# Performance work log

Measured on AMD Instinct MI355X. Metric: run time of the kernel, lower is better.

## Reference

```python
import jax, jax.numpy as jnp
import numpy as np
import math

B, S, E = 4, 2048, 1024

def setup_inputs() -> dict:
    key = jax.random.key(0)
    ks = jax.random.split(key, 12)
    scale = 1.0 / math.sqrt(E)
    inp = {
        "query": jax.random.normal(ks[0], (B, S, E), jnp.float32),
        "key_": jax.random.normal(ks[1], (B, S, E), jnp.float32),
        "value": jax.random.normal(ks[2], (B, S, E), jnp.float32),
        # causal mask, broadcast over batch: 1 = keep, 0 = mask
        "mask": jnp.broadcast_to(jnp.tril(jnp.ones((S, S), jnp.int32)), (B, S, S)),
        "Wq": jax.random.uniform(ks[3], (E, E), jnp.float32, -scale, scale),
        "bq": jax.random.uniform(ks[4], (E,), jnp.float32, -scale, scale),
        "Wk": jax.random.uniform(ks[5], (E, E), jnp.float32, -scale, scale),
        "bk": jax.random.uniform(ks[6], (E,), jnp.float32, -scale, scale),
        "Wv": jax.random.uniform(ks[7], (E, E), jnp.float32, -scale, scale),
        "bv": jax.random.uniform(ks[8], (E,), jnp.float32, -scale, scale),
        "Wo": jax.random.uniform(ks[9], (E, E), jnp.float32, -scale, scale),
        "bo": jax.random.uniform(ks[10], (E,), jnp.float32, -scale, scale),
    }
    return inp

def reference(query, key_, value, mask, Wq, bq, Wk, bk, Wv, bv, Wo, bo):
    # Linear projections (torch Linear: x @ W.T + b)
    Q = jnp.einsum('bse,fe->bsf', query, Wq) + bq
    K = jnp.einsum('bse,fe->bsf', key_, Wk) + bk
    V = jnp.einsum('bse,fe->bsf', value, Wv) + bv
    # NOTE: module never splits heads; scores over full embed_dim, scaled by sqrt(embed_dim)
    scores = jnp.einsum('bqe,bke->bqk', Q, K) / jnp.sqrt(jnp.asarray(E, Q.dtype))
    scores = jnp.where(mask == 0, -jnp.inf, scores)
    attn = jax.nn.softmax(scores, axis=-1)
    attn_out = jnp.einsum('bqk,bke->bqe', attn, V)
    return jnp.einsum('bse,fe->bsf', attn_out, Wo) + bo
```

## Files before the change

### kernel.cpp

```cpp
#include <hip/hip_runtime.h>

typedef __bf16 bf16;
typedef __attribute__((ext_vector_type(8))) __bf16 bf16x8;
typedef __attribute__((ext_vector_type(4))) __bf16 bf16x4;
typedef __attribute__((ext_vector_type(2))) __bf16 bf16x2;
typedef __attribute__((ext_vector_type(4))) float f32x4;

#define DEVINL __device__ __forceinline__

DEVINL void gload_lds16(const bf16* g, bf16* l) {
    __builtin_amdgcn_global_load_lds(
        (__attribute__((address_space(1))) unsigned int*)(unsigned long long)g,
        (__attribute__((address_space(3))) unsigned int*)l,
        16, 0, 0);
}

DEVINL void xcd_swizzle(int& bx, int& by) {
    const int gx = gridDim.x, gy = gridDim.y;
    const int l = blockIdx.y * gx + blockIdx.x;
    const int xcd = l & 7;
    const int li = l >> 3;
    by = xcd * (gy >> 3) + li / gx;
    bx = li - (li / gx) * gx;
}

DEVINL void xcd_swizzle_bal(int& bx, int& by) {
    const int gx = gridDim.x, gy = gridDim.y;
    const int l = blockIdx.y * gx + blockIdx.x;
    const int xcd = l & 7;
    const int li = l >> 3;
    const int j = li / gx;
    bx = li - j * gx;
    by = j ? (gy - 1 - xcd) : xcd;
}

__global__ __launch_bounds__(256) void cvt3_f32_to_bf16(
    const float* __restrict__ a, const float* __restrict__ b,
    const float* __restrict__ c, bf16* __restrict__ out, int n4) {
    int i = blockIdx.x * blockDim.x + threadIdx.x;
    if (i >= n4) return;
    const float* src = (blockIdx.z == 0) ? a : (blockIdx.z == 1) ? b : c;
    bf16* dst = out + (size_t)blockIdx.z * (size_t)n4 * 4;
    float4 f = ((const float4*)src)[i];
    bf16x4 o;
    o.x = (bf16)f.x; o.y = (bf16)f.y; o.z = (bf16)f.z; o.w = (bf16)f.w;
    ((bf16x4*)dst)[i] = o;
}

__global__ __launch_bounds__(256) void cvt4_f32_to_bf16(
    const float* __restrict__ a, const float* __restrict__ b,
    const float* __restrict__ c, const float* __restrict__ d,
    bf16* __restrict__ out, int n4) {
    int i = blockIdx.x * blockDim.x + threadIdx.x;
    if (i >= n4) return;
    const float* src = (blockIdx.z == 0) ? a : (blockIdx.z == 1) ? b
                     : (blockIdx.z == 2) ? c : d;
    bf16* dst = out + (size_t)blockIdx.z * (size_t)n4 * 4;
    float4 f = ((const float4*)src)[i];
    bf16x4 o;
    o.x = (bf16)f.x; o.y = (bf16)f.y; o.z = (bf16)f.z; o.w = (bf16)f.w;
    ((bf16x4*)dst)[i] = o;
}

__global__ __launch_bounds__(256) void transpose_bf16(
    const unsigned short* __restrict__ in, unsigned short* __restrict__ out,
    int R, int C) {
    __shared__ unsigned short t[64][65];
    const size_t bo = (size_t)blockIdx.z * R * C;
    const int r0 = blockIdx.y * 64, c0 = blockIdx.x * 64;
#pragma unroll
    for (int i = 0; i < 16; i++) {
        int lin = threadIdx.x + i * 256;
        int r = lin >> 6, c = lin & 63;
        t[r][c] = in[bo + (size_t)(r0 + r) * C + (c0 + c)];
    }
    __syncthreads();
#pragma unroll
    for (int i = 0; i < 16; i++) {
        int lin = threadIdx.x + i * 256;
        int r = lin >> 6, c = lin & 63;
        out[bo + (size_t)(c0 + r) * R + (r0 + c)] = t[c][r];
    }
}

__global__ __launch_bounds__(256) void bias_fold(
    const float* __restrict__ Wo, const float* __restrict__ bv,
    const float* __restrict__ bo, float* __restrict__ bout) {
    const int e = blockIdx.x * 4 + (threadIdx.x >> 6);
    const int lane = threadIdx.x & 63;
    float s = 0.f;
    for (int k = lane; k < 1024; k += 64) s += Wo[e * 1024 + k] * bv[k];
#pragma unroll
    for (int off = 32; off > 0; off >>= 1) s += __shfl_xor(s, off, 64);
    if (lane == 0) bout[e] = s + bo[e];
}

template <int EPI>
__global__ __launch_bounds__(256) void gemm_bt128(
    const bf16* __restrict__ A, const bf16* __restrict__ B,
    const float* __restrict__ bias0, const float* __restrict__ bias1,
    const float* __restrict__ bias2, void* __restrict__ Cv,
    int M, int N, int K,
    long long sA, long long sB, long long sC,
    float scale) {
    int bx, by;
    xcd_swizzle(bx, by);
    const int bz = blockIdx.z;
    const int m0 = by * 128, n0 = bx * 128;

    A += (size_t)bz * sA;
    B += (size_t)bz * sB;
    const float* bias = (bz == 0) ? bias0 : (bz == 1) ? bias1 : bias2;

    __shared__ __align__(16) bf16 As[2][128 * 32];
    __shared__ __align__(16) bf16 Bs[2][128 * 32];

    const int tid = threadIdx.x;
    const int wave = tid >> 6;
    const int lane = tid & 63;
    const int lr = lane & 15;
    const int lq = lane >> 4;
    const int wm = (wave >> 1) * 64;
    const int wn = (wave & 1) * 64;
    const int srow = lane >> 2;
    const int scol = ((lane & 3) ^ ((lane >> 3) & 3)) * 8;

    const bf16* gA = A + (size_t)(m0 + wave * 16 + srow) * K + scol;
    const bf16* gB = B + (size_t)(n0 + wave * 16 + srow) * K + scol;
    const size_t rowskip = (size_t)64 * K;
    const int rsw = (lq ^ ((lr >> 1) & 3)) * 8;

    f32x4 acc[4][4];
    const f32x4 fzero = {0.f, 0.f, 0.f, 0.f};
#pragma unroll
    for (int i = 0; i < 4; i++)
#pragma unroll
        for (int j = 0; j < 4; j++) acc[i][j] = fzero;

#define STAGE128(bufi)                                          \
    do {                                                        \
        gload_lds16(gA,           As[bufi] + wave * 512);       \
        gload_lds16(gA + rowskip, As[bufi] + (wave + 4) * 512); \
        gload_lds16(gB,           Bs[bufi] + wave * 512);       \
        gload_lds16(gB + rowskip, Bs[bufi] + (wave + 4) * 512); \
        gA += 32; gB += 32;                                     \
    } while (0)

    STAGE128(0);
    int cur = 0;
    for (int k0 = 0; k0 < K; k0 += 32) {
        __syncthreads();
        if (k0 + 32 < K) STAGE128(cur ^ 1);

        bf16x8 af[4], bfr[4];
#pragma unroll
        for (int i = 0; i < 4; i++)
            af[i] = *(const bf16x8*)(As[cur] + (wm + i * 16 + lr) * 32 + rsw);
#pragma unroll
        for (int j = 0; j < 4; j++)
            bfr[j] = *(const bf16x8*)(Bs[cur] + (wn + j * 16 + lr) * 32 + rsw);
#pragma unroll
        for (int i = 0; i < 4; i++)
#pragma unroll
            for (int j = 0; j < 4; j++)
                acc[i][j] = __builtin_amdgcn_mfma_f32_16x16x32_bf16(
                    af[i], bfr[j], acc[i][j], 0, 0, 0);
        cur ^= 1;
    }
#undef STAGE128

#pragma unroll
    for (int j = 0; j < 4; j++) {
        const int col = n0 + wn + j * 16 + lr;
        const float bb = bias ? bias[col] : 0.0f;
#pragma unroll
        for (int i = 0; i < 4; i++) {
            const int rowb = m0 + wm + i * 16 + lq * 4;
#pragma unroll
            for (int r = 0; r < 4; r++) {
                if (EPI == 0)
                    ((bf16*)Cv)[(size_t)bz * sC + (size_t)(rowb + r) * N + col] =
                        (bf16)(acc[i][j][r] * scale + bb);
                else
                    ((float*)Cv)[(size_t)bz * sC + (size_t)(rowb + r) * N + col] =
                        acc[i][j][r] * scale + bb;
            }
        }
    }
}

template <int EPI>
__global__ __launch_bounds__(512) void gemm_pipe(
    const bf16* __restrict__ A, const bf16* __restrict__ B,
    const float* __restrict__ bias0, const float* __restrict__ bias1,
    const float* __restrict__ bias2, void* __restrict__ Cv,
    int M, int N, int K,
    long long sA, long long sB, long long sC,
    float scale, int causal) {
    int bx, by;
    if (causal) xcd_swizzle_bal(bx, by);
    else        xcd_swizzle(bx, by);
    const int bz = blockIdx.z;
    const int m0 = by * 128, n0 = bx * 256;
    if (causal == 1 && n0 > m0 + 127) return;
    const int NT = K >> 5;

    A += (size_t)bz * sA;
    B += (size_t)bz * sB;
    const float* bias = (bz == 0) ? bias0 : (bz == 1) ? bias1 : bias2;

    __shared__ __align__(16) bf16 As[4][128 * 32];
    __shared__ __align__(16) bf16 Bs[4][256 * 32];

    const int tid = threadIdx.x;
    const int wave = tid >> 6;
    const int lane = tid & 63;
    const int lr = lane & 15;
    const int lq = lane >> 4;
    const int wm = (wave >> 2) * 64;
    const int wn = (wave & 3) * 64;

    const int srow = lane >> 2;
    const int scol = ((lane & 3) ^ ((lane >> 3) & 3)) * 8;
    const bf16* gA  = A + (size_t)(m0 + wave * 16 + srow) * K + scol;
    const bf16* gB0 = B + (size_t)(n0 + wave * 32 + srow) * K + scol;
    const size_t rowskip = (size_t)16 * K;

    const int rsw = (lq ^ ((lr >> 1) & 3)) * 8;

    f32x4 acc[4][4];
    const f32x4 fzero = {0.f, 0.f, 0.f, 0.f};
#pragma unroll
    for (int i = 0; i < 4; i++)
#pragma unroll
        for (int j = 0; j < 4; j++) acc[i][j] = fzero;

#define STAGEP(bufi, koff)                                               \
    do {                                                                 \
        gload_lds16(gA + (koff),            As[bufi] + wave * 512);      \
        gload_lds16(gB0 + (koff),           Bs[bufi] + wave * 1024);     \
        gload_lds16(gB0 + rowskip + (koff), Bs[bufi] + wave * 1024 + 512); \
    } while (0)

    STAGEP(0, 0);
    STAGEP(1, 32);
    STAGEP(2, 64);
    asm volatile("s_waitcnt vmcnt(6)" ::: "memory");
    __builtin_amdgcn_s_barrier();

    for (int t = 0; t < NT; ++t) {
        const int bfi = t & 3;

        bf16x8 af[4], bfr[4];
#pragma unroll
        for (int i = 0; i < 4; i++)
            af[i] = *(const bf16x8*)(As[bfi] + (wm + i * 16 + lr) * 32 + rsw);
#pragma unroll
        for (int j = 0; j < 4; j++)
            bfr[j] = *(const bf16x8*)(Bs[bfi] + (wn + j * 16 + lr) * 32 + rsw);

        if (t + 3 < NT) STAGEP((t + 3) & 3, (t + 3) * 32);

        const int rem = NT - 1 - t;
        if (rem >= 3)      asm volatile("s_waitcnt vmcnt(6)" ::: "memory");
        else if (rem == 2) asm volatile("s_waitcnt vmcnt(3)" ::: "memory");
        else if (rem == 1) asm volatile("s_waitcnt vmcnt(0)" ::: "memory");
        __builtin_amdgcn_s_barrier();
        __builtin_amdgcn_sched_barrier(0);

        __builtin_amdgcn_s_setprio(1);
#pragma unroll
        for (int i = 0; i < 4; i++)
#pragma unroll
            for (int j = 0; j < 4; j++)
                acc[i][j] = __builtin_amdgcn_mfma_f32_16x16x32_bf16(
                    af[i], bfr[j], acc[i][j], 0, 0, 0);
        __builtin_amdgcn_s_setprio(0);
        __builtin_amdgcn_s_barrier();
    }
#undef STAGEP

#pragma unroll
    for (int j = 0; j < 4; j++) {
        const int col = n0 + wn + j * 16 + lr;
        const float bb = bias ? bias[col] : 0.0f;
#pragma unroll
        for (int i = 0; i < 4; i++) {
            const int rowb = m0 + wm + i * 16 + lq * 4;
#pragma unroll
            for (int r = 0; r < 4; r++) {
                if (EPI == 0)
                    ((bf16*)Cv)[(size_t)bz * sC + (size_t)(rowb + r) * N + col] =
                        (bf16)(acc[i][j][r] * scale + bb);
                else
                    ((float*)Cv)[(size_t)bz * sC + (size_t)(rowb + r) * N + col] =
                        acc[i][j][r] * scale + bb;
            }
        }
    }
}

__global__ __launch_bounds__(256, 2) void gemm_pv128(
    const bf16* __restrict__ A, const bf16* __restrict__ B,
    const float* __restrict__ bias, float* __restrict__ C,
    int M, int N, int K,
    long long sA, long long sB, long long sC,
    float scale) {
    int bx, by;
    xcd_swizzle_bal(bx, by);
    const int bz = blockIdx.z;
    const int m0 = by * 128, n0 = bx * 128;
    int Keff = m0 + 128; if (Keff > K) Keff = K;
    const int NT = Keff >> 5;

    A += (size_t)bz * sA;
    B += (size_t)bz * sB;

    __shared__ __align__(16) bf16 As[4][128 * 32];
    __shared__ __align__(16) bf16 Bs[4][128 * 32];

    const int tid = threadIdx.x;
    const int wave = tid >> 6;
    const int lane = tid & 63;
    const int lr = lane & 15;
    const int lq = lane >> 4;
    const int wm = (wave >> 1) * 64;
    const int wn = (wave & 1) * 64;

    const int srow = lane >> 2;
    const int scol = ((lane & 3) ^ ((lane >> 3) & 3)) * 8;
    const bf16* gA = A + (size_t)(m0 + wave * 16 + srow) * K + scol;
    const bf16* gB = B + (size_t)(n0 + wave * 16 + srow) * K + scol;
    const size_t rowskip = (size_t)64 * K;

    const int rsw = (lq ^ ((lr >> 1) & 3)) * 8;

    f32x4 acc[4][4];
    const f32x4 fzero = {0.f, 0.f, 0.f, 0.f};
#pragma unroll
    for (int i = 0; i < 4; i++)
#pragma unroll
        for (int j = 0; j < 4; j++) acc[i][j] = fzero;

#define STAGEV(bufi, koff)                                                 \
    do {                                                                   \
        gload_lds16(gA + (koff),           As[bufi] + wave * 512);         \
        gload_lds16(gA + rowskip + (koff), As[bufi] + (wave + 4) * 512);   \
        gload_lds16(gB + (koff),           Bs[bufi] + wave * 512);         \
        gload_lds16(gB + rowskip + (koff), Bs[bufi] + (wave + 4) * 512);   \
    } while (0)

    STAGEV(0, 0);
    STAGEV(1, 32);
    STAGEV(2, 64);
    asm volatile("s_waitcnt vmcnt(8)" ::: "memory");
    __builtin_amdgcn_s_barrier();

    for (int t = 0; t < NT; ++t) {
        const int bfi = t & 3;

        bf16x8 af[4], bfr[4];
#pragma unroll
        for (int i = 0; i < 4; i++)
            af[i] = *(const bf16x8*)(As[bfi] + (wm + i * 16 + lr) * 32 + rsw);
#pragma unroll
        for (int j = 0; j < 4; j++)
            bfr[j] = *(const bf16x8*)(Bs[bfi] + (wn + j * 16 + lr) * 32 + rsw);

        if (t + 3 < NT) STAGEV((t + 3) & 3, (t + 3) * 32);

        const int rem = NT - 1 - t;
        if (rem >= 3)      asm volatile("s_waitcnt vmcnt(8)" ::: "memory");
        else if (rem == 2) asm volatile("s_waitcnt vmcnt(4)" ::: "memory");
        else if (rem == 1) asm volatile("s_waitcnt vmcnt(0)" ::: "memory");
        __builtin_amdgcn_s_barrier();
        __builtin_amdgcn_sched_barrier(0);

        __builtin_amdgcn_s_setprio(1);
#pragma unroll
        for (int i = 0; i < 4; i++)
#pragma unroll
            for (int j = 0; j < 4; j++)
                acc[i][j] = __builtin_amdgcn_mfma_f32_16x16x32_bf16(
                    af[i], bfr[j], acc[i][j], 0, 0, 0);
        __builtin_amdgcn_s_setprio(0);
        __builtin_amdgcn_s_barrier();
    }
#undef STAGEV

#pragma unroll
    for (int j = 0; j < 4; j++) {
        const int col = n0 + wn + j * 16 + lr;
        const float bb = bias[col];
#pragma unroll
        for (int i = 0; i < 4; i++) {
            const int rowb = m0 + wm + i * 16 + lq * 4;
#pragma unroll
            for (int r = 0; r < 4; r++)
                C[(size_t)bz * sC + (size_t)(rowb + r) * N + col] =
                    acc[i][j][r] * scale + bb;
        }
    }
}

__global__ __launch_bounds__(256) void softmax_causal(
    const bf16* __restrict__ Sc, bf16* __restrict__ P, int S) {
    const int row = blockIdx.x;
    const int q = row & (S - 1);
    const bf16* src = Sc + (size_t)row * S;
    bf16* dst = P + (size_t)row * S;
    const int L = q + 1;
    const int tid = threadIdx.x;
    const int k0 = tid * 8;

    bf16x8 u = ((const bf16x8*)src)[tid];
    float v[8];
    float mx = -3.0e38f;
#pragma unroll
    for (int i = 0; i < 8; i++) {
        v[i] = (k0 + i < L) ? (float)u[i] : -3.0e38f;
        mx = fmaxf(mx, v[i]);
    }
#pragma unroll
    for (int off = 32; off > 0; off >>= 1) mx = fmaxf(mx, __shfl_xor(mx, off, 64));
    __shared__ float redm[4], reds[4];
    if ((tid & 63) == 0) redm[tid >> 6] = mx;
    __syncthreads();
    mx = fmaxf(fmaxf(redm[0], redm[1]), fmaxf(redm[2], redm[3]));

    float sum = 0.f;
#pragma unroll
    for (int i = 0; i < 8; i++) {
        float e = (v[i] > -1.0e38f) ? __expf(v[i] - mx) : 0.f;
        v[i] = e;
        sum += e;
    }
#pragma unroll
    for (int off = 32; off > 0; off >>= 1) sum += __shfl_xor(sum, off, 64);
    if ((tid & 63) == 0) reds[tid >> 6] = sum;
    __syncthreads();
    sum = reds[0] + reds[1] + reds[2] + reds[3];
    const float inv = 1.0f / sum;
    bf16x8 o;
#pragma unroll
    for (int i = 0; i < 8; i++) o[i] = (bf16)(v[i] * inv);
    ((bf16x8*)dst)[tid] = o;
}

extern "C" void kernel_launch(void* const* d_in, const int* in_sizes, int n_in,
                              void* d_out, int out_size, void* d_ws, size_t ws_size,
                              hipStream_t stream) {
    const int B = 4, S = 2048, E = 1024;
    const size_t SBE = (size_t)B * S * E;
    const size_t EE = (size_t)E * E;

    const float* q_in = (const float*)d_in[0];
    const float* k_in = (const float*)d_in[1];
    const float* v_in = (const float*)d_in[2];
    const float* Wq = (const float*)d_in[4];
    const float* bq = (const float*)d_in[5];
    const float* Wk = (const float*)d_in[6];
    const float* bk = (const float*)d_in[7];
    const float* Wv = (const float*)d_in[8];
    const float* bv = (const float*)d_in[9];
    const float* Wo = (const float*)d_in[10];
    const float* bo = (const float*)d_in[11];

    char* ws = (char*)d_ws;
    bf16* qkvb = (bf16*)ws;
    bf16* Sc = (bf16*)ws;
    bf16* WvT = (bf16*)(ws + 3 * SBE * 2);
    float* bout = (float*)(ws + 3 * SBE * 2 + EE * 2);
    char* p = ws + (size_t)B * S * S * 4;
    bf16* QKVb = (bf16*)p; p += 3 * SBE * 2;
    bf16* VWt = (bf16*)p; p += SBE * 2;
    bf16* Pb = (bf16*)p; p += (size_t)B * S * S * 2;
    bf16* Wb = (bf16*)p; p += 4 * EE * 2;

    bf16* Qb = QKVb;
    bf16* Kb = QKVb + SBE;
    bf16* VW = QKVb + 2 * SBE;
    bf16* Wob = Wb + 3 * EE;
    bf16* Wvo = Wb + 2 * EE;

    dim3 blk(256), blk512(512);

    dim3 gcvt3((int)(SBE / 4 / 256), 1, 3);
    cvt3_f32_to_bf16<<<gcvt3, blk, 0, stream>>>(q_in, k_in, v_in, qkvb, (int)(SBE / 4));
    dim3 gcvt4((int)(EE / 4 / 256), 1, 4);
    cvt4_f32_to_bf16<<<gcvt4, blk, 0, stream>>>(Wq, Wk, Wv, Wo, Wb, (int)(EE / 4));

    dim3 gtw(16, 16, 1);
    transpose_bf16<<<gtw, blk, 0, stream>>>((const unsigned short*)(Wb + 2 * EE),
                                            (unsigned short*)WvT, E, E);
    dim3 gwvo(E / 128, E / 128, 1);
    gemm_bt128<0><<<gwvo, blk, 0, stream>>>(Wob, WvT, nullptr, nullptr, nullptr,
                                            Wvo, E, E, E, 0, 0, 0, 1.f);
    bias_fold<<<256, blk, 0, stream>>>(Wo, bv, bo, bout);

    dim3 gproj(E / 256, (B * S) / 128, 3);
    gemm_pipe<0><<<gproj, blk512, 0, stream>>>(qkvb, Wb, bq, bk, nullptr, QKVb,
                                               B * S, E, E,
                                               (long long)SBE, (long long)EE,
                                               (long long)SBE, 1.f, 0);

    dim3 gt(E / 64, S / 64, B);
    transpose_bf16<<<gt, blk, 0, stream>>>((const unsigned short*)VW,
                                           (unsigned short*)VWt, S, E);

    dim3 gsc(S / 256, S / 128, B);
    gemm_pipe<0><<<gsc, blk512, 0, stream>>>(Qb, Kb, nullptr, nullptr, nullptr, Sc,
                                             S, S, E,
                                             (long long)S * E, (long long)S * E,
                                             (long long)S * S, 0.03125f, 1);

    softmax_causal<<<B * S, blk, 0, stream>>>(Sc, Pb, S);

    dim3 gpv(E / 128, S / 128, B);
    gemm_pv128<<<gpv, blk, 0, stream>>>(Pb, VWt, bout, (float*)d_out, S, E, S,
                                        (long long)S * S, (long long)E * S,
                                        (long long)S * E, 1.f);
}
```

Baseline: 394.8 us.

## Replace 128x256 GEMM with 256x256 tile, 8-wave ping-pong schedule, vectorize transpose

The projection and score GEMMs move from a 128x256 tile with a 4-stage K=32 pipeline to a 256x256 tile with K=64 double buffering. Each wave now computes a 128x64 sub-tile in quadrant phases, with loads interleaved between barrier-separated MFMA blocks. The aim is more data reuse per LDS byte and better overlap of global-to-LDS copies with MFMA work. The causal launch drops the balanced XCD swizzle, which may hurt load balance, and the larger tile raises register and LDS pressure. The transpose kernel is also changed to use 4-element vector loads and stores.

```diff
diff --git a/kernel.cpp b/kernel.cpp
--- a/kernel.cpp
+++ b/kernel.cpp
@@ -68,18 +68,23 @@
     __shared__ unsigned short t[64][65];
     const size_t bo = (size_t)blockIdx.z * R * C;
     const int r0 = blockIdx.y * 64, c0 = blockIdx.x * 64;
-#pragma unroll
-    for (int i = 0; i < 16; i++) {
-        int lin = threadIdx.x + i * 256;
-        int r = lin >> 6, c = lin & 63;
-        t[r][c] = in[bo + (size_t)(r0 + r) * C + (c0 + c)];
+    const int tr = threadIdx.x >> 4;
+    const int tc = threadIdx.x & 15;
+#pragma unroll
+    for (int i = 0; i < 4; i++) {
+        int r = tr + i * 16;
+        ushort4 v = *(const ushort4*)&in[bo + (size_t)(r0 + r) * C + (c0 + tc * 4)];
+        t[r][tc * 4 + 0] = v.x; t[r][tc * 4 + 1] = v.y;
+        t[r][tc * 4 + 2] = v.z; t[r][tc * 4 + 3] = v.w;
     }
     __syncthreads();
 #pragma unroll
-    for (int i = 0; i < 16; i++) {
-        int lin = threadIdx.x + i * 256;
-        int r = lin >> 6, c = lin & 63;
-        out[bo + (size_t)(c0 + r) * R + (r0 + c)] = t[c][r];
+    for (int i = 0; i < 4; i++) {
+        int r = tr + i * 16;
+        ushort4 v;
+        v.x = t[tc * 4 + 0][r]; v.y = t[tc * 4 + 1][r];
+        v.z = t[tc * 4 + 2][r]; v.w = t[tc * 4 + 3][r];
+        *(ushort4*)&out[bo + (size_t)(c0 + r) * R + (r0 + tc * 4)] = v;
     }
 }
 
@@ -190,7 +195,7 @@
 }
 
 template <int EPI>
-__global__ __launch_bounds__(512) void gemm_pipe(
+__global__ __launch_bounds__(512) void gemm8p(
     const bf16* __restrict__ A, const bf16* __restrict__ B,
     const float* __restrict__ bias0, const float* __restrict__ bias1,
     const float* __restrict__ bias2, void* __restrict__ Cv,
@@ -198,103 +203,166 @@
     long long sA, long long sB, long long sC,
     float scale, int causal) {
     int bx, by;
-    if (causal) xcd_swizzle_bal(bx, by);
+    if (causal) { bx = blockIdx.x; by = blockIdx.y; }
     else        xcd_swizzle(bx, by);
     const int bz = blockIdx.z;
-    const int m0 = by * 128, n0 = bx * 256;
-    if (causal == 1 && n0 > m0 + 127) return;
-    const int NT = K >> 5;
+    const int m0 = by * 256, n0 = bx * 256;
+    if (causal == 1 && n0 > m0 + 255) return;
 
     A += (size_t)bz * sA;
     B += (size_t)bz * sB;
     const float* bias = (bz == 0) ? bias0 : (bz == 1) ? bias1 : bias2;
 
-    __shared__ __align__(16) bf16 As[4][128 * 32];
-    __shared__ __align__(16) bf16 Bs[4][256 * 32];
+    __shared__ __align__(16) bf16 As[2][256 * 64];
+    __shared__ __align__(16) bf16 Bs[2][256 * 64];
 
     const int tid = threadIdx.x;
-    const int wave = tid >> 6;
-    const int lane = tid & 63;
-    const int lr = lane & 15;
-    const int lq = lane >> 4;
-    const int wm = (wave >> 2) * 64;
-    const int wn = (wave & 3) * 64;
-
-    const int srow = lane >> 2;
-    const int scol = ((lane & 3) ^ ((lane >> 3) & 3)) * 8;
-    const bf16* gA  = A + (size_t)(m0 + wave * 16 + srow) * K + scol;
-    const bf16* gB0 = B + (size_t)(n0 + wave * 32 + srow) * K + scol;
-    const size_t rowskip = (size_t)16 * K;
-
-    const int rsw = (lq ^ ((lr >> 1) & 3)) * 8;
-
-    f32x4 acc[4][4];
-    const f32x4 fzero = {0.f, 0.f, 0.f, 0.f};
-#pragma unroll
-    for (int i = 0; i < 4; i++)
-#pragma unroll
-        for (int j = 0; j < 4; j++) acc[i][j] = fzero;
-
-#define STAGEP(bufi, koff)                                               \
-    do {                                                                 \
-        gload_lds16(gA + (koff),            As[bufi] + wave * 512);      \
-        gload_lds16(gB0 + (koff),           Bs[bufi] + wave * 1024);     \
-        gload_lds16(gB0 + rowskip + (koff), Bs[bufi] + wave * 1024 + 512); \
+    const int w  = tid >> 6;
+    const int l  = tid & 63;
+    const int lr = l & 15;
+    const int lq = l >> 4;
+    const int wm = w >> 2;
+    const int wn = w & 3;
+
+    const int x  = lr & 7;
+    const int c0 = ((lq ^ x)) * 8;
+    const int c1 = (((4 | lq) ^ x)) * 8;
+    const int aBase = (wm * 128 + lr) * 64;
+    const int bBase = (wn * 64 + lr) * 64;
+
+    const int srow = w * 8 + (l >> 3);
+    const int scol = ((l & 7) ^ (l >> 3)) * 8;
+    const bf16* gA = A + (size_t)(m0 + srow) * K + scol;
+    const bf16* gB = B + (size_t)(n0 + srow) * K + scol;
+
+    f32x4 acc[8][4];
+    const f32x4 fz = {0.f, 0.f, 0.f, 0.f};
+#pragma unroll
+    for (int i = 0; i < 8; i++)
+#pragma unroll
+        for (int jj = 0; jj < 4; jj++) acc[i][jj] = fz;
+
+    bf16x8 a[8];
+    bf16x8 bb[8];
+
+#define ST_A(b, h, kt)                                                         \
+    do {                                                                       \
+        const bf16* s_ = gA + (size_t)((h) * 128) * K + (size_t)(kt) * 64;     \
+        gload_lds16(s_,                  As[b] + (h) * 8192 + w * 512);        \
+        gload_lds16(s_ + (size_t)64 * K, As[b] + (h) * 8192 + 4096 + w * 512); \
     } while (0)
-
-    STAGEP(0, 0);
-    STAGEP(1, 32);
-    STAGEP(2, 64);
-    asm volatile("s_waitcnt vmcnt(6)" ::: "memory");
-    __builtin_amdgcn_s_barrier();
-
-    for (int t = 0; t < NT; ++t) {
-        const int bfi = t & 3;
-
-        bf16x8 af[4], bfr[4];
-#pragma unroll
-        for (int i = 0; i < 4; i++)
-            af[i] = *(const bf16x8*)(As[bfi] + (wm + i * 16 + lr) * 32 + rsw);
-#pragma unroll
-        for (int j = 0; j < 4; j++)
-            bfr[j] = *(const bf16x8*)(Bs[bfi] + (wn + j * 16 + lr) * 32 + rsw);
-
-        if (t + 3 < NT) STAGEP((t + 3) & 3, (t + 3) * 32);
-
-        const int rem = NT - 1 - t;
-        if (rem >= 3)      asm volatile("s_waitcnt vmcnt(6)" ::: "memory");
-        else if (rem == 2) asm volatile("s_waitcnt vmcnt(3)" ::: "memory");
-        else if (rem == 1) asm volatile("s_waitcnt vmcnt(0)" ::: "memory");
-        __builtin_amdgcn_s_barrier();
-        __builtin_amdgcn_sched_barrier(0);
-
-        __builtin_amdgcn_s_setprio(1);
-#pragma unroll
-        for (int i = 0; i < 4; i++)
-#pragma unroll
-            for (int j = 0; j < 4; j++)
-                acc[i][j] = __builtin_amdgcn_mfma_f32_16x16x32_bf16(
-                    af[i], bfr[j], acc[i][j], 0, 0, 0);
-        __builtin_amdgcn_s_setprio(0);
-        __builtin_amdgcn_s_barrier();
-    }
-#undef STAGEP
-
-#pragma unroll
-    for (int j = 0; j < 4; j++) {
-        const int col = n0 + wn + j * 16 + lr;
-        const float bb = bias ? bias[col] : 0.0f;
-#pragma unroll
-        for (int i = 0; i < 4; i++) {
-            const int rowb = m0 + wm + i * 16 + lq * 4;
-#pragma unroll
-            for (int r = 0; r < 4; r++) {
+#define ST_B(b, h, kt)                                                         \
+    do {                                                                       \
+        const bf16* s_ = gB + (size_t)((h) * 128) * K + (size_t)(kt) * 64;     \
+        gload_lds16(s_,                  Bs[b] + (h) * 8192 + w * 512);        \
+        gload_lds16(s_ + (size_t)64 * K, Bs[b] + (h) * 8192 + 4096 + w * 512); \
+    } while (0)
+#define RD_A(b, q)                                                             \
+    {                                                                          \
+        _Pragma("unroll")                                                      \
+        for (int f = 0; f < 4; ++f) {                                          \
+            a[f * 2 + 0] = *(const bf16x8*)(As[b] + aBase + ((q) * 64 + f * 16) * 64 + c0); \
+            a[f * 2 + 1] = *(const bf16x8*)(As[b] + aBase + ((q) * 64 + f * 16) * 64 + c1); \
+        }                                                                      \
+    }
+#define RD_B(b, p)                                                             \
+    {                                                                          \
+        _Pragma("unroll")                                                      \
+        for (int n = 0; n < 2; ++n) {                                          \
+            bb[((p) * 2 + n) * 2 + 0] = *(const bf16x8*)(Bs[b] + bBase + ((p) * 32 + n * 16) * 64 + c0); \
+            bb[((p) * 2 + n) * 2 + 1] = *(const bf16x8*)(Bs[b] + bBase + ((p) * 32 + n * 16) * 64 + c1); \
+        }                                                                      \
+    }
+#define MM(q, p)                                                               \
+    {                                                                          \
+        __builtin_amdgcn_s_setprio(1);                                         \
+        _Pragma("unroll")                                                      \
+        for (int f = 0; f < 4; ++f) {                                          \
+            _Pragma("unroll")                                                  \
+            for (int n = 0; n < 2; ++n) {                                      \
+                acc[(q) * 4 + f][(p) * 2 + n] = __builtin_amdgcn_mfma_f32_16x16x32_bf16( \
+                    a[f * 2 + 0], bb[((p) * 2 + n) * 2 + 0], acc[(q) * 4 + f][(p) * 2 + n], 0, 0, 0); \
+                acc[(q) * 4 + f][(p) * 2 + n] = __builtin_amdgcn_mfma_f32_16x16x32_bf16( \
+                    a[f * 2 + 1], bb[((p) * 2 + n) * 2 + 1], acc[(q) * 4 + f][(p) * 2 + n], 0, 0, 0); \
+            }                                                                  \
+        }                                                                      \
+        __builtin_amdgcn_s_setprio(0);                                         \
+    }
+#define BAR()                                                                  \
+    {                                                                          \
+        __builtin_amdgcn_sched_barrier(0);                                     \
+        __builtin_amdgcn_s_barrier();                                          \
+        __builtin_amdgcn_sched_barrier(0);                                     \
+    }
+
+    const int NTt = K >> 6;
+    const int NI  = NTt >> 1;
+
+    ST_B(0, 0, 0); ST_B(0, 1, 0);
+    ST_A(0, 0, 0); ST_A(0, 1, 0);
+    ST_B(1, 0, 1); ST_B(1, 1, 1);
+    asm volatile("s_waitcnt vmcnt(4)" ::: "memory");
+    BAR();
+
+    for (int j = 0; j < NI; ++j) {
+        const int vkt = 2 * j + 1, ckt = 2 * j + 2, dkt = 2 * j + 3;
+        const bool dc = ckt < NTt, dd = dkt < NTt;
+
+        RD_A(0, 0) RD_B(0, 0)
+        ST_A(1, 0, vkt);
+        BAR() MM(0, 0) BAR()
+        RD_B(0, 1)
+        ST_A(1, 1, vkt);
+        BAR() MM(0, 1) BAR()
+        RD_A(0, 1)
+        if (dc) ST_B(0, 0, ckt);
+        BAR() MM(1, 1) BAR()
+        if (dc) {
+            ST_B(0, 1, ckt);
+            asm volatile("s_waitcnt vmcnt(4)" ::: "memory");
+        } else {
+            asm volatile("s_waitcnt vmcnt(0)" ::: "memory");
+        }
+        BAR() MM(1, 0) BAR()
+
+        RD_A(1, 0) RD_B(1, 0)
+        if (dc) ST_A(0, 0, ckt);
+        BAR() MM(0, 0) BAR()
+        RD_B(1, 1)
+        if (dc) ST_A(0, 1, ckt);
+        BAR() MM(0, 1) BAR()
+        RD_A(1, 1)
+        if (dd) ST_B(1, 0, dkt);
+        BAR() MM(1, 1) BAR()
+        if (dd) ST_B(1, 1, dkt);
+        if (j + 1 < NI) {
+            if (dd) asm volatile("s_waitcnt vmcnt(4)" ::: "memory");
+            else    asm volatile("s_waitcnt vmcnt(0)" ::: "memory");
+        }
+        BAR() MM(1, 0) BAR()
+    }
+#undef ST_A
+#undef ST_B
+#undef RD_A
+#undef RD_B
+#undef MM
+#undef BAR
+
+#pragma unroll
+    for (int p = 0; p < 4; ++p) {
+        const int col = n0 + wn * 64 + p * 16 + lr;
+        const float bbv = bias ? bias[col] : 0.0f;
+#pragma unroll
+        for (int f = 0; f < 8; ++f) {
+            const int rowb = m0 + wm * 128 + f * 16 + lq * 4;
+#pragma unroll
+            for (int r = 0; r < 4; ++r) {
                 if (EPI == 0)
                     ((bf16*)Cv)[(size_t)bz * sC + (size_t)(rowb + r) * N + col] =
-                        (bf16)(acc[i][j][r] * scale + bb);
+                        (bf16)(acc[f][p][r] * scale + bbv);
                 else
                     ((float*)Cv)[(size_t)bz * sC + (size_t)(rowb + r) * N + col] =
-                        acc[i][j][r] * scale + bb;
+                        acc[f][p][r] * scale + bbv;
             }
         }
     }
@@ -498,21 +566,21 @@
                                             Wvo, E, E, E, 0, 0, 0, 1.f);
     bias_fold<<<256, blk, 0, stream>>>(Wo, bv, bo, bout);
 
-    dim3 gproj(E / 256, (B * S) / 128, 3);
-    gemm_pipe<0><<<gproj, blk512, 0, stream>>>(qkvb, Wb, bq, bk, nullptr, QKVb,
-                                               B * S, E, E,
-                                               (long long)SBE, (long long)EE,
-                                               (long long)SBE, 1.f, 0);
+    dim3 gproj(E / 256, (B * S) / 256, 3);
+    gemm8p<0><<<gproj, blk512, 0, stream>>>(qkvb, Wb, bq, bk, nullptr, QKVb,
+                                            B * S, E, E,
+                                            (long long)SBE, (long long)EE,
+                                            (long long)SBE, 1.f, 0);
 
     dim3 gt(E / 64, S / 64, B);
     transpose_bf16<<<gt, blk, 0, stream>>>((const unsigned short*)VW,
                                            (unsigned short*)VWt, S, E);
 
-    dim3 gsc(S / 256, S / 128, B);
-    gemm_pipe<0><<<gsc, blk512, 0, stream>>>(Qb, Kb, nullptr, nullptr, nullptr, Sc,
-                                             S, S, E,
-                                             (long long)S * E, (long long)S * E,
-                                             (long long)S * S, 0.03125f, 1);
+    dim3 gsc(S / 256, S / 256, B);
+    gemm8p<0><<<gsc, blk512, 0, stream>>>(Qb, Kb, nullptr, nullptr, nullptr, Sc,
+                                          S, S, E,
+                                          (long long)S * E, (long long)S * E,
+                                          (long long)S * S, 0.03125f, 1);
 
     softmax_causal<<<B * S, blk, 0, stream>>>(Sc, Pb, S);
 
```

Measured after the change: 403.3 us. +2.1%, slower.

## Fuse fp32-to-bf16 input conversion into projection GEMM and retile score GEMM

Applied to the files above, without the earlier changes.

Drops the separate conversion kernel for query/key/value and has a new projection GEMM read fp32 activations directly, converting them to bf16 in registers before the LDS store. This removes one full write and re-read of the three bf16 activation tensors. The deep 4-stage 512-thread pipelined GEMM is replaced by simpler double-buffered 256-thread kernels. The score GEMM now uses 128x64 tiles so causal skipping happens at a finer grain. The transpose is vectorised to ushort4, and the workspace layout is reorganised. The risk is that the simpler pipelines, and the synchronous fp32 loads in the projection, hide memory latency less well than the old pipelined kernel.

```diff
diff --git a/kernel.cpp b/kernel.cpp
--- a/kernel.cpp
+++ b/kernel.cpp
@@ -32,19 +32,6 @@
     const int j = li / gx;
     bx = li - j * gx;
     by = j ? (gy - 1 - xcd) : xcd;
-}
-
-__global__ __launch_bounds__(256) void cvt3_f32_to_bf16(
-    const float* __restrict__ a, const float* __restrict__ b,
-    const float* __restrict__ c, bf16* __restrict__ out, int n4) {
-    int i = blockIdx.x * blockDim.x + threadIdx.x;
-    if (i >= n4) return;
-    const float* src = (blockIdx.z == 0) ? a : (blockIdx.z == 1) ? b : c;
-    bf16* dst = out + (size_t)blockIdx.z * (size_t)n4 * 4;
-    float4 f = ((const float4*)src)[i];
-    bf16x4 o;
-    o.x = (bf16)f.x; o.y = (bf16)f.y; o.z = (bf16)f.z; o.w = (bf16)f.w;
-    ((bf16x4*)dst)[i] = o;
 }
 
 __global__ __launch_bounds__(256) void cvt4_f32_to_bf16(
@@ -68,18 +55,23 @@
     __shared__ unsigned short t[64][65];
     const size_t bo = (size_t)blockIdx.z * R * C;
     const int r0 = blockIdx.y * 64, c0 = blockIdx.x * 64;
-#pragma unroll
-    for (int i = 0; i < 16; i++) {
-        int lin = threadIdx.x + i * 256;
-        int r = lin >> 6, c = lin & 63;
-        t[r][c] = in[bo + (size_t)(r0 + r) * C + (c0 + c)];
+    const int tr = threadIdx.x >> 4;
+    const int tc = threadIdx.x & 15;
+#pragma unroll
+    for (int i = 0; i < 4; i++) {
+        int r = tr + i * 16;
+        ushort4 v = *(const ushort4*)&in[bo + (size_t)(r0 + r) * C + (c0 + tc * 4)];
+        t[r][tc * 4 + 0] = v.x; t[r][tc * 4 + 1] = v.y;
+        t[r][tc * 4 + 2] = v.z; t[r][tc * 4 + 3] = v.w;
     }
     __syncthreads();
 #pragma unroll
-    for (int i = 0; i < 16; i++) {
-        int lin = threadIdx.x + i * 256;
-        int r = lin >> 6, c = lin & 63;
-        out[bo + (size_t)(c0 + r) * R + (r0 + c)] = t[c][r];
+    for (int i = 0; i < 4; i++) {
+        int r = tr + i * 16;
+        ushort4 v;
+        v.x = t[tc * 4 + 0][r]; v.y = t[tc * 4 + 1][r];
+        v.z = t[tc * 4 + 2][r]; v.w = t[tc * 4 + 3][r];
+        *(ushort4*)&out[bo + (size_t)(c0 + r) * R + (r0 + tc * 4)] = v;
     }
 }
 
@@ -95,22 +87,12 @@
     if (lane == 0) bout[e] = s + bo[e];
 }
 
-template <int EPI>
 __global__ __launch_bounds__(256) void gemm_bt128(
     const bf16* __restrict__ A, const bf16* __restrict__ B,
-    const float* __restrict__ bias0, const float* __restrict__ bias1,
-    const float* __restrict__ bias2, void* __restrict__ Cv,
-    int M, int N, int K,
-    long long sA, long long sB, long long sC,
-    float scale) {
+    bf16* __restrict__ C, int M, int N, int K) {
     int bx, by;
     xcd_swizzle(bx, by);
-    const int bz = blockIdx.z;
     const int m0 = by * 128, n0 = bx * 128;
-
-    A += (size_t)bz * sA;
-    B += (size_t)bz * sB;
-    const float* bias = (bz == 0) ? bias0 : (bz == 1) ? bias1 : bias2;
 
     __shared__ __align__(16) bf16 As[2][128 * 32];
     __shared__ __align__(16) bf16 Bs[2][128 * 32];
@@ -172,60 +154,48 @@
 #pragma unroll
     for (int j = 0; j < 4; j++) {
         const int col = n0 + wn + j * 16 + lr;
-        const float bb = bias ? bias[col] : 0.0f;
 #pragma unroll
         for (int i = 0; i < 4; i++) {
             const int rowb = m0 + wm + i * 16 + lq * 4;
 #pragma unroll
-            for (int r = 0; r < 4; r++) {
-                if (EPI == 0)
-                    ((bf16*)Cv)[(size_t)bz * sC + (size_t)(rowb + r) * N + col] =
-                        (bf16)(acc[i][j][r] * scale + bb);
-                else
-                    ((float*)Cv)[(size_t)bz * sC + (size_t)(rowb + r) * N + col] =
-                        acc[i][j][r] * scale + bb;
-            }
+            for (int r = 0; r < 4; r++)
+                C[(size_t)(rowb + r) * N + col] = (bf16)acc[i][j][r];
         }
     }
 }
 
-template <int EPI>
-__global__ __launch_bounds__(512) void gemm_pipe(
-    const bf16* __restrict__ A, const bf16* __restrict__ B,
+__global__ __launch_bounds__(256) void gemm_projf(
+    const float* __restrict__ A0, const float* __restrict__ A1,
+    const float* __restrict__ A2, const bf16* __restrict__ Bw,
     const float* __restrict__ bias0, const float* __restrict__ bias1,
-    const float* __restrict__ bias2, void* __restrict__ Cv,
-    int M, int N, int K,
-    long long sA, long long sB, long long sC,
-    float scale, int causal) {
+    bf16* __restrict__ Cq, int M, int N, int K) {
     int bx, by;
-    if (causal) xcd_swizzle_bal(bx, by);
-    else        xcd_swizzle(bx, by);
+    xcd_swizzle(bx, by);
     const int bz = blockIdx.z;
-    const int m0 = by * 128, n0 = bx * 256;
-    if (causal == 1 && n0 > m0 + 127) return;
-    const int NT = K >> 5;
-
-    A += (size_t)bz * sA;
-    B += (size_t)bz * sB;
-    const float* bias = (bz == 0) ? bias0 : (bz == 1) ? bias1 : bias2;
-
-    __shared__ __align__(16) bf16 As[4][128 * 32];
-    __shared__ __align__(16) bf16 Bs[4][256 * 32];
+    const int m0 = by * 128, n0 = bx * 128;
+
+    const float* Af = (bz == 0) ? A0 : (bz == 1) ? A1 : A2;
+    const bf16* B = Bw + (size_t)bz * (size_t)N * K;
+    const float* bias = (bz == 0) ? bias0 : (bz == 1) ? bias1 : nullptr;
+    bf16* C = Cq + (size_t)bz * (size_t)M * N;
+
+    __shared__ __align__(16) bf16 As[2][128 * 32];
+    __shared__ __align__(16) bf16 Bs[2][128 * 32];
 
     const int tid = threadIdx.x;
     const int wave = tid >> 6;
     const int lane = tid & 63;
     const int lr = lane & 15;
     const int lq = lane >> 4;
-    const int wm = (wave >> 2) * 64;
-    const int wn = (wave & 3) * 64;
-
+    const int wm = (wave >> 1) * 64;
+    const int wn = (wave & 1) * 64;
     const int srow = lane >> 2;
-    const int scol = ((lane & 3) ^ ((lane >> 3) & 3)) * 8;
-    const bf16* gA  = A + (size_t)(m0 + wave * 16 + srow) * K + scol;
-    const bf16* gB0 = B + (size_t)(n0 + wave * 32 + srow) * K + scol;
-    const size_t rowskip = (size_t)16 * K;
-
+    const int gsrc = (lane & 3) ^ ((lane >> 3) & 3);
+
+    const float* fA = Af + (size_t)(m0 + wave * 16 + srow) * K + gsrc * 8;
+    const bf16*  gB = B + (size_t)(n0 + wave * 16 + srow) * K + gsrc * 8;
+    const size_t rsA = (size_t)64 * K;
+    const size_t rsB = (size_t)64 * K;
     const int rsw = (lq ^ ((lr >> 1) & 3)) * 8;
 
     f32x4 acc[4][4];
@@ -235,50 +205,50 @@
 #pragma unroll
         for (int j = 0; j < 4; j++) acc[i][j] = fzero;
 
-#define STAGEP(bufi, koff)                                               \
-    do {                                                                 \
-        gload_lds16(gA + (koff),            As[bufi] + wave * 512);      \
-        gload_lds16(gB0 + (koff),           Bs[bufi] + wave * 1024);     \
-        gload_lds16(gB0 + rowskip + (koff), Bs[bufi] + wave * 1024 + 512); \
+#define STGP(bufi)                                                        \
+    do {                                                                  \
+        float4 a00 = *(const float4*)(fA);                                \
+        float4 a01 = *(const float4*)(fA + 4);                            \
+        float4 a10 = *(const float4*)(fA + rsA);                          \
+        float4 a11 = *(const float4*)(fA + rsA + 4);                      \
+        gload_lds16(gB,       Bs[bufi] + wave * 512);                     \
+        gload_lds16(gB + rsB, Bs[bufi] + (wave + 4) * 512);               \
+        bf16x8 p0, p1;                                                    \
+        p0[0] = (bf16)a00.x; p0[1] = (bf16)a00.y;                         \
+        p0[2] = (bf16)a00.z; p0[3] = (bf16)a00.w;                         \
+        p0[4] = (bf16)a01.x; p0[5] = (bf16)a01.y;                         \
+        p0[6] = (bf16)a01.z; p0[7] = (bf16)a01.w;                         \
+        p1[0] = (bf16)a10.x; p1[1] = (bf16)a10.y;                         \
+        p1[2] = (bf16)a10.z; p1[3] = (bf16)a10.w;                         \
+        p1[4] = (bf16)a11.x; p1[5] = (bf16)a11.y;                         \
+        p1[6] = (bf16)a11.z; p1[7] = (bf16)a11.w;                         \
+        *(bf16x8*)(As[bufi] + wave * 512 + lane * 8) = p0;                \
+        *(bf16x8*)(As[bufi] + (wave + 4) * 512 + lane * 8) = p1;          \
+        fA += 32; gB += 32;                                               \
     } while (0)
 
-    STAGEP(0, 0);
-    STAGEP(1, 32);
-    STAGEP(2, 64);
-    asm volatile("s_waitcnt vmcnt(6)" ::: "memory");
-    __builtin_amdgcn_s_barrier();
-
-    for (int t = 0; t < NT; ++t) {
-        const int bfi = t & 3;
+    STGP(0);
+    int cur = 0;
+    for (int k0 = 0; k0 < K; k0 += 32) {
+        __syncthreads();
+        if (k0 + 32 < K) STGP(cur ^ 1);
 
         bf16x8 af[4], bfr[4];
 #pragma unroll
         for (int i = 0; i < 4; i++)
-            af[i] = *(const bf16x8*)(As[bfi] + (wm + i * 16 + lr) * 32 + rsw);
+            af[i] = *(const bf16x8*)(As[cur] + (wm + i * 16 + lr) * 32 + rsw);
 #pragma unroll
         for (int j = 0; j < 4; j++)
-            bfr[j] = *(const bf16x8*)(Bs[bfi] + (wn + j * 16 + lr) * 32 + rsw);
-
-        if (t + 3 < NT) STAGEP((t + 3) & 3, (t + 3) * 32);
-
-        const int rem = NT - 1 - t;
-        if (rem >= 3)      asm volatile("s_waitcnt vmcnt(6)" ::: "memory");
-        else if (rem == 2) asm volatile("s_waitcnt vmcnt(3)" ::: "memory");
-        else if (rem == 1) asm volatile("s_waitcnt vmcnt(0)" ::: "memory");
-        __builtin_amdgcn_s_barrier();
-        __builtin_amdgcn_sched_barrier(0);
-
-        __builtin_amdgcn_s_setprio(1);
+            bfr[j] = *(const bf16x8*)(Bs[cur] + (wn + j * 16 + lr) * 32 + rsw);
 #pragma unroll
         for (int i = 0; i < 4; i++)
 #pragma unroll
             for (int j = 0; j < 4; j++)
                 acc[i][j] = __builtin_amdgcn_mfma_f32_16x16x32_bf16(
                     af[i], bfr[j], acc[i][j], 0, 0, 0);
-        __builtin_amdgcn_s_setprio(0);
-        __builtin_amdgcn_s_barrier();
-    }
-#undef STAGEP
+        cur ^= 1;
+    }
+#undef STGP
 
 #pragma unroll
     for (int j = 0; j < 4; j++) {
@@ -288,16 +258,136 @@
         for (int i = 0; i < 4; i++) {
             const int rowb = m0 + wm + i * 16 + lq * 4;
 #pragma unroll
-            for (int r = 0; r < 4; r++) {
-                if (EPI == 0)
-                    ((bf16*)Cv)[(size_t)bz * sC + (size_t)(rowb + r) * N + col] =
-                        (bf16)(acc[i][j][r] * scale + bb);
-                else
-                    ((float*)Cv)[(size_t)bz * sC + (size_t)(rowb + r) * N + col] =
-                        acc[i][j][r] * scale + bb;
-            }
+            for (int r = 0; r < 4; r++)
+                C[(size_t)(rowb + r) * N + col] = (bf16)(acc[i][j][r] + bb);
         }
     }
+}
+
+__global__ __launch_bounds__(256) void gemm_sc(
+    const bf16* __restrict__ Qb, const bf16* __restrict__ Kb,
+    bf16* __restrict__ Sc, int S, int E) {
+    int bx, by;
+    xcd_swizzle_bal(bx, by);
+    const int bz = blockIdx.z;
+    const int m0 = by * 128, n0 = bx * 64;
+    if (n0 > m0 + 127) return;
+
+    const bf16* A = Qb + (size_t)bz * S * E;
+    const bf16* B = Kb + (size_t)bz * S * E;
+
+    __shared__ __align__(16) bf16 As[2][128 * 32];
+    __shared__ __align__(16) bf16 Bs[2][64 * 32];
+
+    const int tid = threadIdx.x;
+    const int wave = tid >> 6;
+    const int lane = tid & 63;
+    const int lr = lane & 15;
+    const int lq = lane >> 4;
+    const int wm = wave * 32;
+    const int srow = lane >> 2;
+    const int scol = ((lane & 3) ^ ((lane >> 3) & 3)) * 8;
+
+    const bf16* gA = A + (size_t)(m0 + wave * 16 + srow) * E + scol;
+    const bf16* gB = B + (size_t)(n0 + wave * 16 + srow) * E + scol;
+    const size_t rowskip = (size_t)64 * E;
+    const int rsw = (lq ^ ((lr >> 1) & 3)) * 8;
+
+    f32x4 acc[2][4];
+    const f32x4 fzero = {0.f, 0.f, 0.f, 0.f};
+#pragma unroll
+    for (int i = 0; i < 2; i++)
+#pragma unroll
+        for (int j = 0; j < 4; j++) acc[i][j] = fzero;
+
+#define STAGES(bufi)                                            \
+    do {                                                        \
+        gload_lds16(gA,           As[bufi] + wave * 512);       \
+        gload_lds16(gA + rowskip, As[bufi] + (wave + 4) * 512); \
+        gload_lds16(gB,           Bs[bufi] + wave * 512);       \
+        gA += 32; gB += 32;                                     \
+    } while (0)
+
+    STAGES(0);
+    int cur = 0;
+    for (int k0 = 0; k0 < E; k0 += 32) {
+        __syncthreads();
+        if (k0 + 32 < E) STAGES(cur ^ 1);
+
+        bf16x8 af[2], bfr[4];
+#pragma unroll
+        for (int i = 0; i < 2; i++)
+            af[i] = *(const bf16x8*)(As[cur] + (wm + i * 16 + lr) * 32 + rsw);
+#pragma unroll
+        for (int j = 0; j < 4; j++)
+            bfr[j] = *(const bf16x8*)(Bs[cur] + (j * 16 + lr) * 32 + rsw);
+#pragma unroll
+        for (int i = 0; i < 2; i++)
+#pragma unroll
+            for (int j = 0; j < 4; j++)
+                acc[i][j] = __builtin_amdgcn_mfma_f32_16x16x32_bf16(
+                    af[i], bfr[j], acc[i][j], 0, 0, 0);
+        cur ^= 1;
+    }
+#undef STAGES
+
+    bf16* dst = Sc + (size_t)bz * S * S;
+#pragma unroll
+    for (int j = 0; j < 4; j++) {
+        const int col = n0 + j * 16 + lr;
+#pragma unroll
+        for (int i = 0; i < 2; i++) {
+            const int rowb = m0 + wm + i * 16 + lq * 4;
+#pragma unroll
+            for (int r = 0; r < 4; r++)
+                dst[(size_t)(rowb + r) * S + col] =
+                    (bf16)(acc[i][j][r] * 0.03125f);
+        }
+    }
+}
+
+__global__ __launch_bounds__(256) void softmax_causal(
+    const bf16* __restrict__ Sc, bf16* __restrict__ P, int S) {
+    const int row = blockIdx.x;
+    const int q = row & (S - 1);
+    const bf16* src = Sc + (size_t)row * S;
+    bf16* dst = P + (size_t)row * S;
+    const int L = q + 1;
+    const int tid = threadIdx.x;
+    const int k0 = tid * 8;
+
+    bf16x8 u = ((const bf16x8*)src)[tid];
+    float v[8];
+    float mx = -3.0e38f;
+#pragma unroll
+    for (int i = 0; i < 8; i++) {
+        v[i] = (k0 + i < L) ? (float)u[i] : -3.0e38f;
+        mx = fmaxf(mx, v[i]);
+    }
+#pragma unroll
+    for (int off = 32; off > 0; off >>= 1) mx = fmaxf(mx, __shfl_xor(mx, off, 64));
+    __shared__ float redm[4], reds[4];
+    if ((tid & 63) == 0) redm[tid >> 6] = mx;
+    __syncthreads();
+    mx = fmaxf(fmaxf(redm[0], redm[1]), fmaxf(redm[2], redm[3]));
+
+    float sum = 0.f;
+#pragma unroll
+    for (int i = 0; i < 8; i++) {
+        float e = (v[i] > -1.0e38f) ? __expf(v[i] - mx) : 0.f;
+        v[i] = e;
+        sum += e;
+    }
+#pragma unroll
+    for (int off = 32; off > 0; off >>= 1) sum += __shfl_xor(sum, off, 64);
+    if ((tid & 63) == 0) reds[tid >> 6] = sum;
+    __syncthreads();
+    sum = reds[0] + reds[1] + reds[2] + reds[3];
+    const float inv = 1.0f / sum;
+    bf16x8 o;
+#pragma unroll
+    for (int i = 0; i < 8; i++) o[i] = (bf16)(v[i] * inv);
+    ((bf16x8*)dst)[tid] = o;
 }
 
 __global__ __launch_bounds__(256, 2) void gemm_pv128(
@@ -403,56 +493,13 @@
     }
 }
 
-__global__ __launch_bounds__(256) void softmax_causal(
-    const bf16* __restrict__ Sc, bf16* __restrict__ P, int S) {
-    const int row = blockIdx.x;
-    const int q = row & (S - 1);
-    const bf16* src = Sc + (size_t)row * S;
-    bf16* dst = P + (size_t)row * S;
-    const int L = q + 1;
-    const int tid = threadIdx.x;
-    const int k0 = tid * 8;
-
-    bf16x8 u = ((const bf16x8*)src)[tid];
-    float v[8];
-    float mx = -3.0e38f;
-#pragma unroll
-    for (int i = 0; i < 8; i++) {
-        v[i] = (k0 + i < L) ? (float)u[i] : -3.0e38f;
-        mx = fmaxf(mx, v[i]);
-    }
-#pragma unroll
-    for (int off = 32; off > 0; off >>= 1) mx = fmaxf(mx, __shfl_xor(mx, off, 64));
-    __shared__ float redm[4], reds[4];
-    if ((tid & 63) == 0) redm[tid >> 6] = mx;
-    __syncthreads();
-    mx = fmaxf(fmaxf(redm[0], redm[1]), fmaxf(redm[2], redm[3]));
-
-    float sum = 0.f;
-#pragma unroll
-    for (int i = 0; i < 8; i++) {
-        float e = (v[i] > -1.0e38f) ? __expf(v[i] - mx) : 0.f;
-        v[i] = e;
-        sum += e;
-    }
-#pragma unroll
-    for (int off = 32; off > 0; off >>= 1) sum += __shfl_xor(sum, off, 64);
-    if ((tid & 63) == 0) reds[tid >> 6] = sum;
-    __syncthreads();
-    sum = reds[0] + reds[1] + reds[2] + reds[3];
-    const float inv = 1.0f / sum;
-    bf16x8 o;
-#pragma unroll
-    for (int i = 0; i < 8; i++) o[i] = (bf16)(v[i] * inv);
-    ((bf16x8*)dst)[tid] = o;
-}
-
 extern "C" void kernel_launch(void* const* d_in, const int* in_sizes, int n_in,
                               void* d_out, int out_size, void* d_ws, size_t ws_size,
                               hipStream_t stream) {
     const int B = 4, S = 2048, E = 1024;
     const size_t SBE = (size_t)B * S * E;
     const size_t EE = (size_t)E * E;
+    const size_t BSS = (size_t)B * S * S;
 
     const float* q_in = (const float*)d_in[0];
     const float* k_in = (const float*)d_in[1];
@@ -467,15 +514,13 @@
     const float* bo = (const float*)d_in[11];
 
     char* ws = (char*)d_ws;
-    bf16* qkvb = (bf16*)ws;
-    bf16* Sc = (bf16*)ws;
-    bf16* WvT = (bf16*)(ws + 3 * SBE * 2);
-    float* bout = (float*)(ws + 3 * SBE * 2 + EE * 2);
-    char* p = ws + (size_t)B * S * S * 4;
-    bf16* QKVb = (bf16*)p; p += 3 * SBE * 2;
-    bf16* VWt = (bf16*)p; p += SBE * 2;
-    bf16* Pb = (bf16*)p; p += (size_t)B * S * S * 2;
-    bf16* Wb = (bf16*)p; p += 4 * EE * 2;
+    bf16* QKVb = (bf16*)ws;
+    bf16* VWt  = (bf16*)(ws + 3 * SBE * 2);
+    bf16* Sc   = (bf16*)(ws + 4 * SBE * 2);
+    bf16* Pb   = (bf16*)(ws + 4 * SBE * 2 + BSS * 2);
+    bf16* Wb   = (bf16*)(ws + 4 * SBE * 2 + 2 * BSS * 2);
+    bf16* WvT  = Wb + 4 * EE;
+    float* bout = (float*)(WvT + EE);
 
     bf16* Qb = QKVb;
     bf16* Kb = QKVb + SBE;
@@ -483,10 +528,8 @@
     bf16* Wob = Wb + 3 * EE;
     bf16* Wvo = Wb + 2 * EE;
 
-    dim3 blk(256), blk512(512);
-
-    dim3 gcvt3((int)(SBE / 4 / 256), 1, 3);
-    cvt3_f32_to_bf16<<<gcvt3, blk, 0, stream>>>(q_in, k_in, v_in, qkvb, (int)(SBE / 4));
+    dim3 blk(256);
+
     dim3 gcvt4((int)(EE / 4 / 256), 1, 4);
     cvt4_f32_to_bf16<<<gcvt4, blk, 0, stream>>>(Wq, Wk, Wv, Wo, Wb, (int)(EE / 4));
 
@@ -494,25 +537,19 @@
     transpose_bf16<<<gtw, blk, 0, stream>>>((const unsigned short*)(Wb + 2 * EE),
                                             (unsigned short*)WvT, E, E);
     dim3 gwvo(E / 128, E / 128, 1);
-    gemm_bt128<0><<<gwvo, blk, 0, stream>>>(Wob, WvT, nullptr, nullptr, nullptr,
-                                            Wvo, E, E, E, 0, 0, 0, 1.f);
+    gemm_bt128<<<gwvo, blk, 0, stream>>>(Wob, WvT, Wvo, E, E, E);
     bias_fold<<<256, blk, 0, stream>>>(Wo, bv, bo, bout);
 
-    dim3 gproj(E / 256, (B * S) / 128, 3);
-    gemm_pipe<0><<<gproj, blk512, 0, stream>>>(qkvb, Wb, bq, bk, nullptr, QKVb,
-                                               B * S, E, E,
-                                               (long long)SBE, (long long)EE,
-                                               (long long)SBE, 1.f, 0);
+    dim3 gproj(E / 128, (B * S) / 128, 3);
+    gemm_projf<<<gproj, blk, 0, stream>>>(q_in, k_in, v_in, Wb, bq, bk,
+                                          QKVb, B * S, E, E);
 
     dim3 gt(E / 64, S / 64, B);
     transpose_bf16<<<gt, blk, 0, stream>>>((const unsigned short*)VW,
                                            (unsigned short*)VWt, S, E);
 
-    dim3 gsc(S / 256, S / 128, B);
-    gemm_pipe<0><<<gsc, blk512, 0, stream>>>(Qb, Kb, nullptr, nullptr, nullptr, Sc,
-                                             S, S, E,
-                                             (long long)S * E, (long long)S * E,
-                                             (long long)S * S, 0.03125f, 1);
+    dim3 gsc(S / 64, S / 128, B);
+    gemm_sc<<<gsc, blk, 0, stream>>>(Qb, Kb, Sc, S, E);
 
     softmax_causal<<<B * S, blk, 0, stream>>>(Sc, Pb, S);
 
```

Result: slower. 429.4 us (+8.8%).
